# Performance work log

Measured on AMD Instinct MI355X. Metric: run time of the kernel, lower is better.

The kernel has to match this reference:

```python
import jax, jax.numpy as jnp
import numpy as np

B, S, H = 2, 2048, 1024
NUM_HEAD = 16
HEAD_HIDDEN = H // NUM_HEAD
SCALE = float(np.sqrt(HEAD_HIDDEN))  # 8.0
INF = 10000000000.0


def setup_inputs() -> dict:
    key = jax.random.key(0)
    ks = jax.random.split(key, 12)
    std = 1.0 / np.sqrt(H)
    mk = lambda k: (jax.random.normal(k, (H, H), jnp.float32) * std)
    return {
        "query": jax.random.normal(ks[0], (B, S, H), jnp.float32),
        "key": jax.random.normal(ks[1], (B, S, H), jnp.float32),
        "value": jax.random.normal(ks[2], (B, S, H), jnp.float32),
        "att_mask": jnp.ones((B, 1, 1, S), jnp.float32),
        "wq": mk(ks[3]), "bq": jnp.zeros((H,), jnp.float32),
        "wk": mk(ks[4]), "bk": jnp.zeros((H,), jnp.float32),
        "wv": mk(ks[5]), "bv": jnp.zeros((H,), jnp.float32),
        "wo": mk(ks[6]), "bo": jnp.zeros((H,), jnp.float32),
    }


def reference(query, key, value, att_mask, wq, bq, wk, bk, wv, bv, wo, bo):
    # projections (weights stored as [in, out])
    q = query @ wq + bq
    k = key @ wk + bk
    v = value @ wv + bv
    # split heads: [B, S, nH, hd]
    q = q.reshape(B, S, NUM_HEAD, HEAD_HIDDEN)
    k = k.reshape(B, S, NUM_HEAD, HEAD_HIDDEN)
    v = v.reshape(B, S, NUM_HEAD, HEAD_HIDDEN)
    # scores [B, nH, Sq, Sk], first divide by scale
    att = jnp.einsum("bqhd,bkhd->bhqk", q, k) / SCALE
    # additive mask applied BEFORE the second scale division (faithful quirk)
    att = att + (1.0 - att_mask) * (-INF)
    att = jax.nn.softmax(att / SCALE, axis=-1)
    out = jnp.einsum("bhqk,bkhd->bqhd", att, v).reshape(B, S, H)
    return out @ wo + bo
```

## Files before the change

kernel.cpp:

```cpp
#include <hip/hip_runtime.h>
#include <cstdint>

typedef unsigned short u16;
typedef __attribute__((ext_vector_type(8))) short bf16x8;
typedef __attribute__((ext_vector_type(4))) short bf16x4;
typedef __attribute__((ext_vector_type(4))) float f32x4;

#define S_LEN 2048
#define HDIM  1024
#define NHEAD 16

__device__ __forceinline__ float bf2f(u16 u){ return __uint_as_float(((uint32_t)u) << 16); }
__device__ __forceinline__ u16 f2bf(float f){
  uint32_t x = __float_as_uint(f);
  return (u16)((x + 0x7fffu + ((x >> 16) & 1u)) >> 16);
}

__device__ __forceinline__ float exp2_fast(float x){
  float r; asm("v_exp_f32 %0, %1" : "=v"(r) : "v"(x)); return r;
}

__device__ __forceinline__ void gload_lds16(const void* g, void* l){
  __builtin_amdgcn_global_load_lds((const __attribute__((address_space(1))) void*)g,
                                   (__attribute__((address_space(3))) void*)l, 16, 0, 0);
}

__device__ __forceinline__ int xcd_swz(int d, int n){
  int cpx = n >> 3;
  return (d & 7) * cpx + (d >> 3);
}

__global__ __launch_bounds__(256) void k_cvt3(const float* __restrict__ q, const float* __restrict__ k,
                                              const float* __restrict__ v, u16* __restrict__ oq,
                                              u16* __restrict__ ok, u16* __restrict__ ov){
  int z = blockIdx.y;
  const float* in = z == 0 ? q : (z == 1 ? k : v);
  u16* out = z == 0 ? oq : (z == 1 ? ok : ov);
  int i = blockIdx.x * 256 + threadIdx.x;
  float4 f0 = *(const float4*)&in[(size_t)i * 8];
  float4 f1 = *(const float4*)&in[(size_t)i * 8 + 4];
  bf16x8 o;
  o[0] = (short)f2bf(f0.x); o[1] = (short)f2bf(f0.y);
  o[2] = (short)f2bf(f0.z); o[3] = (short)f2bf(f0.w);
  o[4] = (short)f2bf(f1.x); o[5] = (short)f2bf(f1.y);
  o[6] = (short)f2bf(f1.z); o[7] = (short)f2bf(f1.w);
  *(bf16x8*)&out[(size_t)i * 8] = o;
}

__global__ __launch_bounds__(256) void k_tr_w4(const float* __restrict__ w0, const float* __restrict__ w1,
                                               const float* __restrict__ w2, const float* __restrict__ w3,
                                               u16* __restrict__ o0, u16* __restrict__ o1,
                                               u16* __restrict__ o2, u16* __restrict__ o3){
  int z = blockIdx.z;
  const float* in = z == 0 ? w0 : (z == 1 ? w1 : (z == 2 ? w2 : w3));
  u16* out = z == 0 ? o0 : (z == 1 ? o1 : (z == 2 ? o2 : o3));
  __shared__ float t[64][65];
  int r0 = threadIdx.x >> 6;
  int c  = threadIdx.x & 63;
  int bx = blockIdx.x * 64, by = blockIdx.y * 64;
  #pragma unroll
  for (int i = 0; i < 64; i += 4) t[r0 + i][c] = in[(size_t)(by + r0 + i) * 1024 + bx + c];
  __syncthreads();
  #pragma unroll
  for (int i = 0; i < 64; i += 4) out[(size_t)(bx + r0 + i) * 1024 + by + c] = f2bf(t[c][r0 + i]);
}

__global__ __launch_bounds__(256) void k_tr_v(const u16* __restrict__ v, u16* __restrict__ vt){
  __shared__ u16 t[64][65];
  int r0 = threadIdx.x >> 6, c = threadIdx.x & 63;
  int s0 = blockIdx.x * 64;
  int bh = blockIdx.y;
  int b = bh >> 4, h = bh & 15;
  const u16* src = v + (size_t)b * S_LEN * HDIM + h * 64;
  #pragma unroll
  for (int i = 0; i < 64; i += 4) t[r0 + i][c] = src[(size_t)(s0 + r0 + i) * HDIM + c];
  __syncthreads();
  u16* dst = vt + (size_t)bh * 64 * S_LEN + s0;
  #pragma unroll
  for (int i = 0; i < 64; i += 4) dst[(size_t)(r0 + i) * S_LEN + c] = t[c][r0 + i];
}

__global__ __launch_bounds__(256) void k_gemm_qkv(const u16* __restrict__ A0, const u16* __restrict__ A1,
                                                  const u16* __restrict__ A2,
                                                  const u16* __restrict__ W0, const u16* __restrict__ W1,
                                                  const u16* __restrict__ W2,
                                                  const float* __restrict__ b0, const float* __restrict__ b1,
                                                  const float* __restrict__ b2,
                                                  u16* __restrict__ C0, u16* __restrict__ C1,
                                                  u16* __restrict__ C2)
{
  int d = blockIdx.x + 32 * (blockIdx.y + 8 * blockIdx.z);
  int L = xcd_swz(d, 768);
  int yb = L & 7, xb = (L >> 3) & 31, z = L >> 8;

  const u16* A  = z == 0 ? A0 : (z == 1 ? A1 : A2);
  const u16* Wt = z == 0 ? W0 : (z == 1 ? W1 : W2);
  const float* bias = z == 0 ? b0 : (z == 1 ? b1 : b2);
  u16* C = z == 0 ? C0 : (z == 1 ? C1 : C2);
  float scale = z == 0 ? (1.44269504f / 64.0f) : 1.0f;

  __shared__ u16 As[2][128 * 32];
  __shared__ u16 Bs[2][128 * 32];
  const int K = 1024, N = 1024;
  int tid = threadIdx.x;
  int lane = tid & 63, wave = tid >> 6;
  int quad = lane >> 4, c16 = lane & 15;
  int wm = wave >> 1, wn = wave & 1;
  int m0 = xb * 128, n0 = yb * 128;

  auto stageAB = [&](int k0, int bb) {
    #pragma unroll
    for (int i = 0; i < 2; i++) {
      int slot = tid + i * 256;
      int r = slot >> 2, cc = (slot & 3) * 8;
      gload_lds16(&A [(size_t)(m0 + r) * K + k0 + cc], &As[bb][slot * 8]);
      gload_lds16(&Wt[(size_t)(n0 + r) * K + k0 + cc], &Bs[bb][slot * 8]);
    }
  };

  f32x4 acc[4][4] = {};

  stageAB(0, 0);
  __syncthreads();

  for (int k0 = 0; k0 < K; k0 += 32) {
    int cb = (k0 >> 5) & 1;
    if (k0 + 32 < K) stageAB(k0 + 32, cb ^ 1);
    bf16x8 af[4], bfr[4];
    #pragma unroll
    for (int mt = 0; mt < 4; mt++) af[mt]  = *(const bf16x8*)&As[cb][(wm * 64 + mt * 16 + c16) * 32 + quad * 8];
    #pragma unroll
    for (int nt = 0; nt < 4; nt++) bfr[nt] = *(const bf16x8*)&Bs[cb][(wn * 64 + nt * 16 + c16) * 32 + quad * 8];
    #pragma unroll
    for (int mt = 0; mt < 4; mt++)
      #pragma unroll
      for (int nt = 0; nt < 4; nt++)
        acc[mt][nt] = __builtin_amdgcn_mfma_f32_16x16x32_bf16(af[mt], bfr[nt], acc[mt][nt], 0, 0, 0);
    __syncthreads();
  }

  #pragma unroll
  for (int nt = 0; nt < 4; nt++) {
    int gc = n0 + wn * 64 + nt * 16 + c16;
    float bv = bias[gc];
    #pragma unroll
    for (int mt = 0; mt < 4; mt++)
      #pragma unroll
      for (int r = 0; r < 4; r++) {
        int gr = m0 + wm * 64 + mt * 16 + quad * 4 + r;
        C[(size_t)gr * N + gc] = f2bf((acc[mt][nt][r] + bv) * scale);
      }
  }
}

__global__ __launch_bounds__(256) void k_gemm_o(const u16* __restrict__ A, const u16* __restrict__ Wt,
                                                const float* __restrict__ bias, float* __restrict__ C)
{
  int d = blockIdx.x + 32 * blockIdx.y;
  int L = xcd_swz(d, 512);
  int yb = L & 15, xb = L >> 4;

  __shared__ u16 As[2][128 * 32];
  __shared__ u16 Bs[2][64 * 32];
  const int K = 1024, N = 1024;
  int tid = threadIdx.x;
  int lane = tid & 63, wave = tid >> 6;
  int quad = lane >> 4, c16 = lane & 15;
  int wm = wave >> 1, wn = wave & 1;
  int m0 = xb * 128, n0 = yb * 64;

  auto stageAB = [&](int k0, int bb) {
    #pragma unroll
    for (int i = 0; i < 2; i++) {
      int slot = tid + i * 256;
      int r = slot >> 2, cc = (slot & 3) * 8;
      gload_lds16(&A[(size_t)(m0 + r) * K + k0 + cc], &As[bb][slot * 8]);
    }
    {
      int r = tid >> 2, cc = (tid & 3) * 8;
      gload_lds16(&Wt[(size_t)(n0 + r) * K + k0 + cc], &Bs[bb][tid * 8]);
    }
  };

  f32x4 acc[4][2] = {};

  stageAB(0, 0);
  __syncthreads();

  for (int k0 = 0; k0 < K; k0 += 32) {
    int cb = (k0 >> 5) & 1;
    if (k0 + 32 < K) stageAB(k0 + 32, cb ^ 1);
    bf16x8 af[4], bfr[2];
    #pragma unroll
    for (int mt = 0; mt < 4; mt++) af[mt]  = *(const bf16x8*)&As[cb][(wm * 64 + mt * 16 + c16) * 32 + quad * 8];
    #pragma unroll
    for (int nt = 0; nt < 2; nt++) bfr[nt] = *(const bf16x8*)&Bs[cb][(wn * 32 + nt * 16 + c16) * 32 + quad * 8];
    #pragma unroll
    for (int mt = 0; mt < 4; mt++)
      #pragma unroll
      for (int nt = 0; nt < 2; nt++)
        acc[mt][nt] = __builtin_amdgcn_mfma_f32_16x16x32_bf16(af[mt], bfr[nt], acc[mt][nt], 0, 0, 0);
    __syncthreads();
  }

  #pragma unroll
  for (int nt = 0; nt < 2; nt++) {
    int gc = n0 + wn * 32 + nt * 16 + c16;
    float bv = bias[gc];
    #pragma unroll
    for (int mt = 0; mt < 4; mt++)
      #pragma unroll
      for (int r = 0; r < 4; r++) {
        int gr = m0 + wm * 64 + mt * 16 + quad * 4 + r;
        C[(size_t)gr * N + gc] = acc[mt][nt][r] + bv;
      }
  }
}

__global__ __launch_bounds__(256, 2) void k_attn(const u16* __restrict__ Qm,
                                                 const u16* __restrict__ Km,
                                                 const u16* __restrict__ VTm,
                                                 const float* __restrict__ mask,
                                                 u16* __restrict__ Om)
{
  __shared__ u16 KV[2][9216];
  __shared__ float Msall[S_LEN];
  const int NT = S_LEN / 64;
  int tid = threadIdx.x;
  int lane = tid & 63, wave = tid >> 6;
  int quad = lane >> 4, c16 = lane & 15;
  int wq = wave >> 1, wkv = wave & 1;

  int d = blockIdx.x + 16 * (blockIdx.y + 16 * blockIdx.z);
  int L = xcd_swz(d, 512);
  int qb = L & 15, h = (L >> 4) & 15, b = L >> 8;

  const size_t SH = (size_t)S_LEN * HDIM;
  const u16* Qbase  = Qm + (size_t)b * SH + (size_t)qb * 128 * HDIM + h * 64;
  const u16* Kbase  = Km + (size_t)b * SH + h * 64;
  const u16* VTbase = VTm + (size_t)(b * NHEAD + h) * 64 * S_LEN;
  const float* Mbase = mask + (size_t)b * S_LEN;

  auto stage = [&](int s0, int bb) {
    #pragma unroll
    for (int i = 0; i < 5; i++) {
      int c = i * 256 + tid;
      if (c < 576) {
        int r = c / 9, cc = c - r * 9;
        int col = (cc == 8) ? 0 : cc * 8;
        gload_lds16(&Kbase[(size_t)(s0 + r) * HDIM + col], &KV[bb][c * 8]);
      } else if (c < 1152) {
        int c2 = c - 576;
        int r = c2 / 9, cc = c2 - r * 9;
        int col = (cc == 8) ? 0 : cc * 8;
        gload_lds16(&VTbase[(size_t)r * S_LEN + s0 + col], &KV[bb][4608 + c2 * 8]);
      }
    }
  };

  stage(0, 0);
  for (int i = tid; i < S_LEN; i += 256) Msall[i] = (1.0f - Mbase[i]) * (-1.8033688e9f);

  int qw0 = wq * 64;
  int kv0 = wkv * 32;

  bf16x8 bq[4][2];
  #pragma unroll
  for (int qt = 0; qt < 4; qt++)
    #pragma unroll
    for (int kk = 0; kk < 2; kk++)
      bq[qt][kk] = *(const bf16x8*)&Qbase[(size_t)(qw0 + qt * 16 + c16) * HDIM + kk * 32 + quad * 8];

  f32x4 oacc[4][4] = {};
  float lsq[4] = {};

  __syncthreads();

  for (int kt = 0; kt < NT; kt++) {
    int s0 = kt * 64;
    int cb = kt & 1;
    const u16* Kb = &KV[cb][0];
    const u16* Vb = &KV[cb][4608];
    if (kt + 1 < NT) stage(s0 + 64, cb ^ 1);

    f32x4 madd[2];
    #pragma unroll
    for (int kv2 = 0; kv2 < 2; kv2++) madd[kv2] = *(const f32x4*)&Msall[s0 + kv0 + kv2 * 16 + quad * 4];

    bf16x8 ak0[2], ak1[2];
    #pragma unroll
    for (int kv2 = 0; kv2 < 2; kv2++) {
      ak0[kv2] = *(const bf16x8*)&Kb[(kv0 + kv2 * 16 + c16) * 72 + quad * 8];
      ak1[kv2] = *(const bf16x8*)&Kb[(kv0 + kv2 * 16 + c16) * 72 + 32 + quad * 8];
    }
    f32x4 sacc[2][4];
    __builtin_amdgcn_s_setprio(1);
    #pragma unroll
    for (int kv2 = 0; kv2 < 2; kv2++)
      #pragma unroll
      for (int qt = 0; qt < 4; qt++)
        sacc[kv2][qt] = __builtin_amdgcn_mfma_f32_16x16x32_bf16(ak0[kv2], bq[qt][0], madd[kv2], 0, 0, 0);
    #pragma unroll
    for (int kv2 = 0; kv2 < 2; kv2++)
      #pragma unroll
      for (int qt = 0; qt < 4; qt++)
        sacc[kv2][qt] = __builtin_amdgcn_mfma_f32_16x16x32_bf16(ak1[kv2], bq[qt][1], sacc[kv2][qt], 0, 0, 0);
    __builtin_amdgcn_s_setprio(0);

    bf16x4 pa[4][2];
    #pragma unroll
    for (int kv2 = 0; kv2 < 2; kv2++)
      #pragma unroll
      for (int qt = 0; qt < 4; qt++) {
        float p0 = exp2_fast(sacc[kv2][qt][0]);
        float p1 = exp2_fast(sacc[kv2][qt][1]);
        float p2 = exp2_fast(sacc[kv2][qt][2]);
        float p3 = exp2_fast(sacc[kv2][qt][3]);
        lsq[qt] += (p0 + p1) + (p2 + p3);
        union { uint32_t u[2]; bf16x4 v; } cv;
        asm("v_cvt_pk_bf16_f32 %0, %1, %2" : "=v"(cv.u[0]) : "v"(p0), "v"(p1));
        asm("v_cvt_pk_bf16_f32 %0, %1, %2" : "=v"(cv.u[1]) : "v"(p2), "v"(p3));
        pa[qt][kv2] = cv.v;
      }

    __builtin_amdgcn_s_setprio(1);
    #pragma unroll
    for (int kv2 = 0; kv2 < 2; kv2++) {
      bf16x4 vb[4];
      #pragma unroll
      for (int dt = 0; dt < 4; dt++)
        vb[dt] = *(const bf16x4*)&Vb[(dt * 16 + c16) * 72 + kv0 + kv2 * 16 + quad * 4];
      #pragma unroll
      for (int qt = 0; qt < 4; qt++)
        #pragma unroll
        for (int dt = 0; dt < 4; dt++)
          oacc[qt][dt] = __builtin_amdgcn_mfma_f32_16x16x16bf16_1k(pa[qt][kv2], vb[dt], oacc[qt][dt], 0, 0, 0);
    }
    __builtin_amdgcn_s_setprio(0);
    __syncthreads();
  }

  #pragma unroll
  for (int qt = 0; qt < 4; qt++) {
    float v = lsq[qt];
    v += __shfl_xor(v, 16);
    v += __shfl_xor(v, 32);
    lsq[qt] = v;
  }

  float* Osc = (float*)&KV[0][0];
  float* Lsc = Msall;
  if (wkv == 1) {
    float* Ob = Osc + wq * 4096;
    #pragma unroll
    for (int qt = 0; qt < 4; qt++)
      #pragma unroll
      for (int dt = 0; dt < 4; dt++)
        #pragma unroll
        for (int r = 0; r < 4; r++)
          Ob[(qt * 16 + quad * 4 + r) * 64 + dt * 16 + c16] = oacc[qt][dt][r];
    if (lane < 16)
      #pragma unroll
      for (int qt = 0; qt < 4; qt++) Lsc[wq * 64 + qt * 16 + lane] = lsq[qt];
  }
  __syncthreads();
  if (wkv == 0) {
    float* Ob = Osc + wq * 4096;
    u16* Obase = Om + (size_t)b * SH + (size_t)qb * 128 * HDIM + h * 64;
    #pragma unroll
    for (int qt = 0; qt < 4; qt++)
      #pragma unroll
      for (int r = 0; r < 4; r++) {
        float l = __shfl(lsq[qt], quad * 4 + r) + Lsc[wq * 64 + qt * 16 + quad * 4 + r];
        float rinv = 1.0f / l;
        int lr = qw0 + qt * 16 + quad * 4 + r;
        #pragma unroll
        for (int dt = 0; dt < 4; dt++) {
          float o = oacc[qt][dt][r] + Ob[(qt * 16 + quad * 4 + r) * 64 + dt * 16 + c16];
          Obase[(size_t)lr * HDIM + dt * 16 + c16] = f2bf(o * rinv);
        }
      }
  }
}

extern "C" void kernel_launch(void* const* d_in, const int* in_sizes, int n_in,
                              void* d_out, int out_size, void* d_ws, size_t ws_size,
                              hipStream_t stream)
{
  (void)in_sizes; (void)n_in; (void)out_size; (void)ws_size;
  const float* q_in = (const float*)d_in[0];
  const float* k_in = (const float*)d_in[1];
  const float* v_in = (const float*)d_in[2];
  const float* mask = (const float*)d_in[3];
  const float* wq   = (const float*)d_in[4];
  const float* bq   = (const float*)d_in[5];
  const float* wk   = (const float*)d_in[6];
  const float* bk   = (const float*)d_in[7];
  const float* wv   = (const float*)d_in[8];
  const float* bv   = (const float*)d_in[9];
  const float* wo   = (const float*)d_in[10];
  const float* bo   = (const float*)d_in[11];

  u16* ws  = (u16*)d_ws;
  u16* wqt = ws;
  u16* wkt = wqt + (1u << 20);
  u16* wvt = wkt + (1u << 20);
  u16* wot = wvt + (1u << 20);
  u16* qi_ = wot + (1u << 20);
  u16* ki_ = qi_ + (4u << 20);
  u16* vi_ = ki_ + (4u << 20);
  u16* qb_ = vi_ + (4u << 20);
  u16* kb_ = qb_ + (4u << 20);
  u16* vb_ = kb_ + (4u << 20);
  u16* vtb = vb_ + (4u << 20);
  u16* ob_ = vtb + (4u << 20);

  dim3 blk(256);
  k_cvt3<<<dim3(2048, 3), blk, 0, stream>>>(q_in, k_in, v_in, qi_, ki_, vi_);
  k_tr_w4<<<dim3(16, 16, 4), blk, 0, stream>>>(wq, wk, wv, wo, wqt, wkt, wvt, wot);
  k_gemm_qkv<<<dim3(32, 8, 3), blk, 0, stream>>>(qi_, ki_, vi_, wqt, wkt, wvt, bq, bk, bv, qb_, kb_, vb_);
  k_tr_v<<<dim3(32, 32), blk, 0, stream>>>(vb_, vtb);
  k_attn<<<dim3(16, 16, 2), blk, 0, stream>>>(qb_, kb_, vtb, mask, ob_);
  k_gemm_o<<<dim3(32, 16), blk, 0, stream>>>(ob_, wot, bo, (float*)d_out);
}
```

Measured before the change: 227.2 us.

## Split attention KV tile across four waves per query group using 512-thread blocks

The attention kernel now runs 512 threads (8 waves), with each pair of query waves splitting the 64-key tile four ways (16 keys per wave) instead of two. Per-wave register state for scores and probabilities shrinks, and more waves per CU are available to hide LDS and exp latency. The staging loop is redistributed across the larger block. The cost is a longer serial reduction of partial outputs through LDS at the end, with three store/accumulate rounds each separated by barriers, plus more waves contending at every per-tile barrier.

Measured after the change: 263.6 us. 16.0% more time.

```diff
diff --git a/kernel.cpp b/kernel.cpp
--- a/kernel.cpp
+++ b/kernel.cpp
@@ -217,7 +217,7 @@
   }
 }
 
-__global__ __launch_bounds__(256, 2) void k_attn(const u16* __restrict__ Qm,
+__global__ __launch_bounds__(512, 4) void k_attn(const u16* __restrict__ Qm,
                                                  const u16* __restrict__ Km,
                                                  const u16* __restrict__ VTm,
                                                  const float* __restrict__ mask,
@@ -229,7 +229,7 @@
   int tid = threadIdx.x;
   int lane = tid & 63, wave = tid >> 6;
   int quad = lane >> 4, c16 = lane & 15;
-  int wq = wave >> 1, wkv = wave & 1;
+  int wq = wave >> 2, wkv = wave & 3;
 
   int d = blockIdx.x + 16 * (blockIdx.y + 16 * blockIdx.z);
   int L = xcd_swz(d, 512);
@@ -242,27 +242,38 @@
   const float* Mbase = mask + (size_t)b * S_LEN;
 
   auto stage = [&](int s0, int bb) {
-    #pragma unroll
-    for (int i = 0; i < 5; i++) {
-      int c = i * 256 + tid;
+    {
+      int c = tid;
+      int r = c / 9, cc = c - r * 9;
+      int col = (cc == 8) ? 0 : cc * 8;
+      gload_lds16(&Kbase[(size_t)(s0 + r) * HDIM + col], &KV[bb][c * 8]);
+    }
+    {
+      int c = 512 + tid;
       if (c < 576) {
         int r = c / 9, cc = c - r * 9;
         int col = (cc == 8) ? 0 : cc * 8;
         gload_lds16(&Kbase[(size_t)(s0 + r) * HDIM + col], &KV[bb][c * 8]);
-      } else if (c < 1152) {
+      } else {
         int c2 = c - 576;
         int r = c2 / 9, cc = c2 - r * 9;
         int col = (cc == 8) ? 0 : cc * 8;
         gload_lds16(&VTbase[(size_t)r * S_LEN + s0 + col], &KV[bb][4608 + c2 * 8]);
       }
     }
+    if (tid < 128) {
+      int c2 = 448 + tid;
+      int r = c2 / 9, cc = c2 - r * 9;
+      int col = (cc == 8) ? 0 : cc * 8;
+      gload_lds16(&VTbase[(size_t)r * S_LEN + s0 + col], &KV[bb][4608 + c2 * 8]);
+    }
   };
 
   stage(0, 0);
-  for (int i = tid; i < S_LEN; i += 256) Msall[i] = (1.0f - Mbase[i]) * (-1.8033688e9f);
+  for (int i = tid; i < S_LEN; i += 512) Msall[i] = (1.0f - Mbase[i]) * (-1.8033688e9f);
 
   int qw0 = wq * 64;
-  int kv0 = wkv * 32;
+  int kv0 = wkv * 16;
 
   bf16x8 bq[4][2];
   #pragma unroll
@@ -283,58 +294,45 @@
     const u16* Vb = &KV[cb][4608];
     if (kt + 1 < NT) stage(s0 + 64, cb ^ 1);
 
-    f32x4 madd[2];
-    #pragma unroll
-    for (int kv2 = 0; kv2 < 2; kv2++) madd[kv2] = *(const f32x4*)&Msall[s0 + kv0 + kv2 * 16 + quad * 4];
-
-    bf16x8 ak0[2], ak1[2];
-    #pragma unroll
-    for (int kv2 = 0; kv2 < 2; kv2++) {
-      ak0[kv2] = *(const bf16x8*)&Kb[(kv0 + kv2 * 16 + c16) * 72 + quad * 8];
-      ak1[kv2] = *(const bf16x8*)&Kb[(kv0 + kv2 * 16 + c16) * 72 + 32 + quad * 8];
-    }
-    f32x4 sacc[2][4];
+    f32x4 madd = *(const f32x4*)&Msall[s0 + kv0 + quad * 4];
+
+    bf16x8 ak0 = *(const bf16x8*)&Kb[(kv0 + c16) * 72 + quad * 8];
+    bf16x8 ak1 = *(const bf16x8*)&Kb[(kv0 + c16) * 72 + 32 + quad * 8];
+    f32x4 sacc[4];
     __builtin_amdgcn_s_setprio(1);
     #pragma unroll
-    for (int kv2 = 0; kv2 < 2; kv2++)
-      #pragma unroll
-      for (int qt = 0; qt < 4; qt++)
-        sacc[kv2][qt] = __builtin_amdgcn_mfma_f32_16x16x32_bf16(ak0[kv2], bq[qt][0], madd[kv2], 0, 0, 0);
-    #pragma unroll
-    for (int kv2 = 0; kv2 < 2; kv2++)
-      #pragma unroll
-      for (int qt = 0; qt < 4; qt++)
-        sacc[kv2][qt] = __builtin_amdgcn_mfma_f32_16x16x32_bf16(ak1[kv2], bq[qt][1], sacc[kv2][qt], 0, 0, 0);
+    for (int qt = 0; qt < 4; qt++)
+      sacc[qt] = __builtin_amdgcn_mfma_f32_16x16x32_bf16(ak0, bq[qt][0], madd, 0, 0, 0);
+    #pragma unroll
+    for (int qt = 0; qt < 4; qt++)
+      sacc[qt] = __builtin_amdgcn_mfma_f32_16x16x32_bf16(ak1, bq[qt][1], sacc[qt], 0, 0, 0);
     __builtin_amdgcn_s_setprio(0);
 
-    bf16x4 pa[4][2];
-    #pragma unroll
-    for (int kv2 = 0; kv2 < 2; kv2++)
-      #pragma unroll
-      for (int qt = 0; qt < 4; qt++) {
-        float p0 = exp2_fast(sacc[kv2][qt][0]);
-        float p1 = exp2_fast(sacc[kv2][qt][1]);
-        float p2 = exp2_fast(sacc[kv2][qt][2]);
-        float p3 = exp2_fast(sacc[kv2][qt][3]);
-        lsq[qt] += (p0 + p1) + (p2 + p3);
-        union { uint32_t u[2]; bf16x4 v; } cv;
-        asm("v_cvt_pk_bf16_f32 %0, %1, %2" : "=v"(cv.u[0]) : "v"(p0), "v"(p1));
-        asm("v_cvt_pk_bf16_f32 %0, %1, %2" : "=v"(cv.u[1]) : "v"(p2), "v"(p3));
-        pa[qt][kv2] = cv.v;
-      }
+    bf16x4 pa[4];
+    #pragma unroll
+    for (int qt = 0; qt < 4; qt++) {
+      float p0 = exp2_fast(sacc[qt][0]);
+      float p1 = exp2_fast(sacc[qt][1]);
+      float p2 = exp2_fast(sacc[qt][2]);
+      float p3 = exp2_fast(sacc[qt][3]);
+      lsq[qt] += (p0 + p1) + (p2 + p3);
+      union { uint32_t u[2]; bf16x4 v; } cv;
+      asm("v_cvt_pk_bf16_f32 %0, %1, %2" : "=v"(cv.u[0]) : "v"(p0), "v"(p1));
+      asm("v_cvt_pk_bf16_f32 %0, %1, %2" : "=v"(cv.u[1]) : "v"(p2), "v"(p3));
+      pa[qt] = cv.v;
+    }
 
     __builtin_amdgcn_s_setprio(1);
-    #pragma unroll
-    for (int kv2 = 0; kv2 < 2; kv2++) {
+    {
       bf16x4 vb[4];
       #pragma unroll
       for (int dt = 0; dt < 4; dt++)
-        vb[dt] = *(const bf16x4*)&Vb[(dt * 16 + c16) * 72 + kv0 + kv2 * 16 + quad * 4];
+        vb[dt] = *(const bf16x4*)&Vb[(dt * 16 + c16) * 72 + kv0 + quad * 4];
       #pragma unroll
       for (int qt = 0; qt < 4; qt++)
         #pragma unroll
         for (int dt = 0; dt < 4; dt++)
-          oacc[qt][dt] = __builtin_amdgcn_mfma_f32_16x16x16bf16_1k(pa[qt][kv2], vb[dt], oacc[qt][dt], 0, 0, 0);
+          oacc[qt][dt] = __builtin_amdgcn_mfma_f32_16x16x16bf16_1k(pa[qt], vb[dt], oacc[qt][dt], 0, 0, 0);
     }
     __builtin_amdgcn_s_setprio(0);
     __syncthreads();
@@ -350,35 +348,52 @@
 
   float* Osc = (float*)&KV[0][0];
   float* Lsc = Msall;
-  if (wkv == 1) {
-    float* Ob = Osc + wq * 4096;
+  float* Ob = Osc + wq * 4096;
+
+  if (lane < 16)
+    #pragma unroll
+    for (int qt = 0; qt < 4; qt++) Lsc[((wkv * 2 + wq) * 4 + qt) * 16 + lane] = lsq[qt];
+
+  #pragma unroll
+  for (int src = 1; src < 4; src++) {
+    if (wkv == src) {
+      #pragma unroll
+      for (int qt = 0; qt < 4; qt++)
+        #pragma unroll
+        for (int dt = 0; dt < 4; dt++)
+          #pragma unroll
+          for (int r = 0; r < 4; r++)
+            Ob[(qt * 16 + quad * 4 + r) * 64 + dt * 16 + c16] = oacc[qt][dt][r];
+    }
+    __syncthreads();
+    if (wkv == 0) {
+      #pragma unroll
+      for (int qt = 0; qt < 4; qt++)
+        #pragma unroll
+        for (int dt = 0; dt < 4; dt++)
+          #pragma unroll
+          for (int r = 0; r < 4; r++)
+            oacc[qt][dt][r] += Ob[(qt * 16 + quad * 4 + r) * 64 + dt * 16 + c16];
+    }
+    __syncthreads();
+  }
+
+  if (wkv == 0) {
+    u16* Obase = Om + (size_t)b * SH + (size_t)qb * 128 * HDIM + h * 64;
     #pragma unroll
     for (int qt = 0; qt < 4; qt++)
       #pragma unroll
-      for (int dt = 0; dt < 4; dt++)
+      for (int r = 0; r < 4; r++) {
+        int qrow = quad * 4 + r;
+        float l = Lsc[(0 * 2 + wq) * 4 * 16 + qt * 16 + qrow]
+                + Lsc[(1 * 2 + wq) * 4 * 16 + qt * 16 + qrow]
+                + Lsc[(2 * 2 + wq) * 4 * 16 + qt * 16 + qrow]
+                + Lsc[(3 * 2 + wq) * 4 * 16 + qt * 16 + qrow];
+        float rinv = 1.0f / l;
+        int lr = qw0 + qt * 16 + qrow;
         #pragma unroll
-        for (int r = 0; r < 4; r++)
-          Ob[(qt * 16 + quad * 4 + r) * 64 + dt * 16 + c16] = oacc[qt][dt][r];
-    if (lane < 16)
-      #pragma unroll
-      for (int qt = 0; qt < 4; qt++) Lsc[wq * 64 + qt * 16 + lane] = lsq[qt];
-  }
-  __syncthreads();
-  if (wkv == 0) {
-    float* Ob = Osc + wq * 4096;
-    u16* Obase = Om + (size_t)b * SH + (size_t)qb * 128 * HDIM + h * 64;
-    #pragma unroll
-    for (int qt = 0; qt < 4; qt++)
-      #pragma unroll
-      for (int r = 0; r < 4; r++) {
-        float l = __shfl(lsq[qt], quad * 4 + r) + Lsc[wq * 64 + qt * 16 + quad * 4 + r];
-        float rinv = 1.0f / l;
-        int lr = qw0 + qt * 16 + quad * 4 + r;
-        #pragma unroll
-        for (int dt = 0; dt < 4; dt++) {
-          float o = oacc[qt][dt][r] + Ob[(qt * 16 + quad * 4 + r) * 64 + dt * 16 + c16];
-          Obase[(size_t)lr * HDIM + dt * 16 + c16] = f2bf(o * rinv);
-        }
+        for (int dt = 0; dt < 4; dt++)
+          Obase[(size_t)lr * HDIM + dt * 16 + c16] = f2bf(oacc[qt][dt][r] * rinv);
       }
   }
 }
@@ -420,6 +435,6 @@
   k_tr_w4<<<dim3(16, 16, 4), blk, 0, stream>>>(wq, wk, wv, wo, wqt, wkt, wvt, wot);
   k_gemm_qkv<<<dim3(32, 8, 3), blk, 0, stream>>>(qi_, ki_, vi_, wqt, wkt, wvt, bq, bk, bv, qb_, kb_, vb_);
   k_tr_v<<<dim3(32, 32), blk, 0, stream>>>(vb_, vtb);
-  k_attn<<<dim3(16, 16, 2), blk, 0, stream>>>(qb_, kb_, vtb, mask, ob_);
+  k_attn<<<dim3(16, 16, 2), dim3(512), 0, stream>>>(qb_, kb_, vtb, mask, ob_);
   k_gemm_o<<<dim3(32, 16), blk, 0, stream>>>(ob_, wot, bo, (float*)d_out);
 }
```
